# Kernel tuning notes

Measured on AMD Instinct MI355X. Metric: run time of the kernel, lower is better.

## Reference

```python
import jax, jax.numpy as jnp
import numpy as np

MEMORY_SIZE = 512
EMBED_DIM = 768
BATCH, SEQ = 4, 8192


def setup_inputs() -> dict:
    key = jax.random.key(0)
    k1, k2 = jax.random.split(key)
    hidden_states = jax.random.normal(k1, (BATCH, SEQ, EMBED_DIM), dtype=jnp.float32)
    memory = jax.random.normal(k2, (MEMORY_SIZE, EMBED_DIM), dtype=jnp.float32)
    return {"hidden_states": hidden_states, "memory": memory}


def reference(hidden_states, memory):
    # importance[s] = mean over batch of L2 norm of hidden_states[b, s, :]
    importance = jnp.linalg.norm(hidden_states, axis=-1).mean(axis=0)  # [S]
    k = min(MEMORY_SIZE, importance.shape[0])  # static
    _, topk_idx = jax.lax.top_k(importance, k)  # [k]
    # gather per-token batch-mean vectors and scatter into first k memory slots
    mean_h = hidden_states.mean(axis=0)  # [S, D]
    new_memory = memory.at[:k].set(mean_h[topk_idx])  # [M, D]
    return new_memory
```

## Files before the change

kernel.cpp:

```cpp
#include <hip/hip_runtime.h>
#include <stdint.h>

#define S_TOK 8192
#define D_DIM 768
#define B_SZ  4
#define K_TOP 512
#define NSLICE 32
#define SLICE (S_TOK / NSLICE)

__global__ __launch_bounds__(256) void importance_kernel(const float4* __restrict__ h4,
                                                         uint32_t* __restrict__ imp_u) {
    const int D4 = D_DIM / 4;
    int wave = (blockIdx.x * blockDim.x + threadIdx.x) >> 6;
    int lane = threadIdx.x & 63;
    if (wave >= S_TOK) return;
    float acc = 0.f;
#pragma unroll
    for (int b = 0; b < B_SZ; ++b) {
        const float4* row = h4 + ((size_t)b * S_TOK + (size_t)wave) * D4;
        float ss = 0.f;
#pragma unroll
        for (int j = 0; j < 3; ++j) {
            float4 v = row[lane + 64 * j];
            ss += v.x * v.x + v.y * v.y + v.z * v.z + v.w * v.w;
        }
#pragma unroll
        for (int off = 32; off >= 1; off >>= 1) ss += __shfl_xor(ss, off);
        acc += sqrtf(ss);
    }
    if (lane == 0) imp_u[wave] = __float_as_uint(acc * 0.25f);
}

__global__ __launch_bounds__(256) void rank_kernel(const uint32_t* __restrict__ imp_u,
                                                   uint32_t* __restrict__ partial) {
    const int grp = blockIdx.x >> 5;
    const int c   = blockIdx.x & 31;
    const int s   = grp * 256 + threadIdx.x;
    const uint32_t ks = imp_u[s];
    const uint4* slice4 = (const uint4*)(imp_u + c * SLICE);
    uint32_t cnt = 0;
#pragma unroll 8
    for (int j4 = 0; j4 < SLICE / 4; ++j4) {
        uint4 kv = slice4[j4];
        const int jb = c * SLICE + j4 * 4;
        cnt += (kv.x > ks || (kv.x == ks && (jb + 0) < s)) ? 1u : 0u;
        cnt += (kv.y > ks || (kv.y == ks && (jb + 1) < s)) ? 1u : 0u;
        cnt += (kv.z > ks || (kv.z == ks && (jb + 2) < s)) ? 1u : 0u;
        cnt += (kv.w > ks || (kv.w == ks && (jb + 3) < s)) ? 1u : 0u;
    }
    partial[c * S_TOK + s] = cnt;
}

__global__ __launch_bounds__(64) void sum_gather_kernel(const uint32_t* __restrict__ partial,
                                                        const float4* __restrict__ h4,
                                                        float4* __restrict__ out4) {
    const int s = blockIdx.x;
    const int lane = threadIdx.x;
    uint32_t v = (lane < NSLICE) ? partial[lane * S_TOK + s] : 0u;
#pragma unroll
    for (int off = 16; off >= 1; off >>= 1) v += __shfl_down(v, off);
    const int rank = (int)__shfl(v, 0);
    if (rank >= K_TOP) return;

    const int D4 = D_DIM / 4;
    const size_t SD4 = (size_t)S_TOK * D4;
    const float4* base = h4 + (size_t)s * D4;
#pragma unroll
    for (int j = 0; j < 3; ++j) {
        int d = lane + 64 * j;
        float4 a = base[d];
        float4 b = base[d + SD4];
        float4 c = base[d + 2 * SD4];
        float4 e = base[d + 3 * SD4];
        float4 r;
        r.x = 0.25f * (a.x + b.x + c.x + e.x);
        r.y = 0.25f * (a.y + b.y + c.y + e.y);
        r.z = 0.25f * (a.z + b.z + c.z + e.z);
        r.w = 0.25f * (a.w + b.w + c.w + e.w);
        out4[(size_t)rank * D4 + d] = r;
    }
}

extern "C" void kernel_launch(void* const* d_in, const int* in_sizes, int n_in,
                              void* d_out, int out_size, void* d_ws, size_t ws_size,
                              hipStream_t stream) {
    const float* h = (const float*)d_in[0];
    float* out = (float*)d_out;
    uint32_t* imp_u = (uint32_t*)d_ws;
    uint32_t* partial = (uint32_t*)((char*)d_ws + S_TOK * sizeof(uint32_t));

    importance_kernel<<<S_TOK / 4, 256, 0, stream>>>((const float4*)h, imp_u);
    rank_kernel<<<NSLICE * (S_TOK / 256), 256, 0, stream>>>(imp_u, partial);
    sum_gather_kernel<<<S_TOK, 64, 0, stream>>>(partial, (const float4*)h, (float4*)out);
}
```

Baseline: 39.44 us.

## Split rank-sum from gather and parallelize importance across batch waves

The importance kernel now gives each token one block of four waves, one wave per batch row, and combines the per-batch norms through shared memory. The old fused sum+gather kernel launched 8192 blocks, most of which exited early. It is replaced by a small kernel that sums the partial ranks and writes a rank-to-token map, followed by a gather kernel with exactly 512 blocks. This removes the mostly idle launches but adds an extra kernel launch and a global round-trip for the map.

New measurement: 40.65 us. 1.03x slower.

```diff
diff --git a/kernel.cpp b/kernel.cpp
--- a/kernel.cpp
+++ b/kernel.cpp
@@ -11,24 +11,27 @@
 __global__ __launch_bounds__(256) void importance_kernel(const float4* __restrict__ h4,
                                                          uint32_t* __restrict__ imp_u) {
     const int D4 = D_DIM / 4;
-    int wave = (blockIdx.x * blockDim.x + threadIdx.x) >> 6;
-    int lane = threadIdx.x & 63;
-    if (wave >= S_TOK) return;
-    float acc = 0.f;
+    const int s = blockIdx.x;
+    const int b = threadIdx.x >> 6;
+    const int lane = threadIdx.x & 63;
+    __shared__ float s_red[B_SZ];
+
+    const float4* row = h4 + ((size_t)b * S_TOK + (size_t)s) * D4;
+    float4 v0 = row[lane];
+    float4 v1 = row[lane + 64];
+    float4 v2 = row[lane + 128];
+    float ss = 0.f;
+    ss += v0.x * v0.x + v0.y * v0.y + v0.z * v0.z + v0.w * v0.w;
+    ss += v1.x * v1.x + v1.y * v1.y + v1.z * v1.z + v1.w * v1.w;
+    ss += v2.x * v2.x + v2.y * v2.y + v2.z * v2.z + v2.w * v2.w;
 #pragma unroll
-    for (int b = 0; b < B_SZ; ++b) {
-        const float4* row = h4 + ((size_t)b * S_TOK + (size_t)wave) * D4;
-        float ss = 0.f;
-#pragma unroll
-        for (int j = 0; j < 3; ++j) {
-            float4 v = row[lane + 64 * j];
-            ss += v.x * v.x + v.y * v.y + v.z * v.z + v.w * v.w;
-        }
-#pragma unroll
-        for (int off = 32; off >= 1; off >>= 1) ss += __shfl_xor(ss, off);
-        acc += sqrtf(ss);
+    for (int off = 32; off >= 1; off >>= 1) ss += __shfl_xor(ss, off);
+    if (lane == 0) s_red[b] = ss;
+    __syncthreads();
+    if (threadIdx.x == 0) {
+        float acc = sqrtf(s_red[0]) + sqrtf(s_red[1]) + sqrtf(s_red[2]) + sqrtf(s_red[3]);
+        imp_u[s] = __float_as_uint(acc * 0.25f);
     }
-    if (lane == 0) imp_u[wave] = __float_as_uint(acc * 0.25f);
 }
 
 __global__ __launch_bounds__(256) void rank_kernel(const uint32_t* __restrict__ imp_u,
@@ -51,34 +54,33 @@
     partial[c * S_TOK + s] = cnt;
 }
 
-__global__ __launch_bounds__(64) void sum_gather_kernel(const uint32_t* __restrict__ partial,
-                                                        const float4* __restrict__ h4,
-                                                        float4* __restrict__ out4) {
-    const int s = blockIdx.x;
-    const int lane = threadIdx.x;
-    uint32_t v = (lane < NSLICE) ? partial[lane * S_TOK + s] : 0u;
+__global__ __launch_bounds__(256) void summap_kernel(const uint32_t* __restrict__ partial,
+                                                     int* __restrict__ map) {
+    const int s = blockIdx.x * 256 + threadIdx.x;
+    uint32_t r = 0;
 #pragma unroll
-    for (int off = 16; off >= 1; off >>= 1) v += __shfl_down(v, off);
-    const int rank = (int)__shfl(v, 0);
-    if (rank >= K_TOP) return;
+    for (int c = 0; c < NSLICE; ++c) r += partial[c * S_TOK + s];
+    if (r < K_TOP) map[r] = s;
+}
 
+__global__ __launch_bounds__(192) void gather_kernel(const float4* __restrict__ h4,
+                                                     const int* __restrict__ map,
+                                                     float4* __restrict__ out4) {
     const int D4 = D_DIM / 4;
     const size_t SD4 = (size_t)S_TOK * D4;
-    const float4* base = h4 + (size_t)s * D4;
-#pragma unroll
-    for (int j = 0; j < 3; ++j) {
-        int d = lane + 64 * j;
-        float4 a = base[d];
-        float4 b = base[d + SD4];
-        float4 c = base[d + 2 * SD4];
-        float4 e = base[d + 3 * SD4];
-        float4 r;
-        r.x = 0.25f * (a.x + b.x + c.x + e.x);
-        r.y = 0.25f * (a.y + b.y + c.y + e.y);
-        r.z = 0.25f * (a.z + b.z + c.z + e.z);
-        r.w = 0.25f * (a.w + b.w + c.w + e.w);
-        out4[(size_t)rank * D4 + d] = r;
-    }
+    const int idx = map[blockIdx.x];
+    const float4* base = h4 + (size_t)idx * D4;
+    const int d = threadIdx.x;
+    float4 a = base[d];
+    float4 b = base[d + SD4];
+    float4 c = base[d + 2 * SD4];
+    float4 e = base[d + 3 * SD4];
+    float4 r;
+    r.x = 0.25f * (a.x + b.x + c.x + e.x);
+    r.y = 0.25f * (a.y + b.y + c.y + e.y);
+    r.z = 0.25f * (a.z + b.z + c.z + e.z);
+    r.w = 0.25f * (a.w + b.w + c.w + e.w);
+    out4[(size_t)blockIdx.x * D4 + d] = r;
 }
 
 extern "C" void kernel_launch(void* const* d_in, const int* in_sizes, int n_in,
@@ -88,8 +90,10 @@
     float* out = (float*)d_out;
     uint32_t* imp_u = (uint32_t*)d_ws;
     uint32_t* partial = (uint32_t*)((char*)d_ws + S_TOK * sizeof(uint32_t));
+    int* map = (int*)((char*)d_ws + S_TOK * sizeof(uint32_t) + NSLICE * S_TOK * sizeof(uint32_t));
 
-    importance_kernel<<<S_TOK / 4, 256, 0, stream>>>((const float4*)h, imp_u);
+    importance_kernel<<<S_TOK, 256, 0, stream>>>((const float4*)h, imp_u);
     rank_kernel<<<NSLICE * (S_TOK / 256), 256, 0, stream>>>(imp_u, partial);
-    sum_gather_kernel<<<S_TOK, 64, 0, stream>>>(partial, (const float4*)h, (float4*)out);
+    summap_kernel<<<S_TOK / 256, 256, 0, stream>>>(partial, map);
+    gather_kernel<<<K_TOP, 192, 0, stream>>>((const float4*)h, map, (float4*)out);
 }
```
